# Kernel optimization log

Hardware: AMD Instinct MI355X
Metric: run time of the kernel (lower is better)

## Reference

```python
import jax, jax.numpy as jnp
import numpy as np

N_NODES = 256
IN_FEATURES = 4096
OUT_FEATURES = 7
LAYERS = 4
WIRES = 8                      # ceil(log2(n_nodes))
DIM = 2 ** WIRES               # state-vector length = 256
P2 = WIRES * (WIRES - 1) // 2  # 28 controlled gates per block
N_W = 6 * WIRES + 3 * P2       # 132 weights per layer (matches weight_shape)
CPLX = jnp.complex64
# op2_all_layers ordering: gaps 1..w-1, then j
PAIRS = [(j, j + gap) for gap in range(1, WIRES) for j in range(WIRES - gap)]


def _ry(t):
    c, s = jnp.cos(t / 2), jnp.sin(t / 2)
    return jnp.stack([jnp.stack([c, -s]), jnp.stack([s, c])]).astype(CPLX)


def _rx(t):
    c = jnp.cos(t / 2).astype(CPLX)
    s = (-1j * jnp.sin(t / 2)).astype(CPLX)
    return jnp.stack([jnp.stack([c, s]), jnp.stack([s, c])])


def _rz(t):
    z = jnp.zeros((), CPLX)
    return jnp.stack([jnp.stack([jnp.exp(-0.5j * t).astype(CPLX), z]),
                      jnp.stack([z, jnp.exp(0.5j * t).astype(CPLX)])])


# Constant-angle gates (the source passes the integer weight index as the
# controlled-rotation angle, so these are compile-time numpy constants).
def _ry_np(a):
    c, s = np.cos(a / 2), np.sin(a / 2)
    return np.array([[c, -s], [s, c]], np.complex64)


def _rx_np(a):
    c, s = np.cos(a / 2), np.sin(a / 2)
    return np.array([[c, -1j * s], [-1j * s, c]], np.complex64)


def _rz_np(a):
    return np.diag([np.exp(-0.5j * a), np.exp(0.5j * a)]).astype(np.complex64)


def apply_1q(state, M, q):
    # state: [B] + [2]*WIRES; wire q lives on axis q+1 (wire 0 = MSB, PennyLane order)
    s = jnp.moveaxis(state, q + 1, -1)
    s = jnp.einsum('...b,ab->...a', s, M)
    return jnp.moveaxis(s, -1, q + 1)


def apply_c1q(state, M, c, t):
    # controlled gate: apply M on target wire t in the control==1 subspace
    s = jnp.moveaxis(state, (c + 1, t + 1), (-2, -1))
    s1 = jnp.einsum('...b,ab->...a', s[..., 1, :], M)
    s = jnp.stack([s[..., 0, :], s1], axis=-2)
    return jnp.moveaxis(s, (-2, -1), (c + 1, t + 1))


def q_layer(state, wv):
    # Faithful port of the source q_layer, including the quirk that the
    # CRY/CRX/CRZ angles are the integer running weight index (constants).
    wi = 0
    for q in range(WIRES):
        state = apply_1q(state, _ry(wv[wi + q]), q)
    wi += WIRES
    for i, (c, t) in enumerate(PAIRS):
        state = apply_c1q(state, _ry_np(float(wi + i)), c, t)
    wi += P2
    for q in range(WIRES):
        state = apply_1q(state, _ry(wv[wi + q]), q)
    wi += WIRES
    for q in range(WIRES):
        state = apply_1q(state, _rx(wv[wi + q]), q)
    wi += WIRES
    for i, (c, t) in enumerate(PAIRS):
        state = apply_c1q(state, _rx_np(float(wi + i)), c, t)
    wi += P2
    for q in range(WIRES):
        state = apply_1q(state, _rx(wv[wi + q]), q)
    wi += WIRES
    for q in range(WIRES):
        state = apply_1q(state, _rz(wv[wi + q]), q)
    wi += WIRES
    for i, (c, t) in enumerate(PAIRS):
        state = apply_c1q(state, _rz_np(float(wi + i)), c, t)
    wi += P2
    for q in range(WIRES):
        state = apply_1q(state, _rz(wv[wi + q]), q)
    return state


def circuit(samples, qweights):
    # samples: [B, N_NODES] real -> AmplitudeEmbedding(pad_with=0, normalize=True)
    B = samples.shape[0]
    v = samples
    if DIM > N_NODES:
        v = jnp.pad(v, ((0, 0), (0, DIM - N_NODES)))
    v = v / jnp.linalg.norm(v, axis=1, keepdims=True)
    state = v.astype(CPLX).reshape((B,) + (2,) * WIRES)
    layer = jax.checkpoint(q_layer)  # bounds residual memory under AD
    for l in range(LAYERS):
        state = layer(state, qweights[l])
    p = state.real ** 2 + state.imag ** 2  # probabilities, [B] + [2]*WIRES
    zs = []
    for q in range(WIRES):
        axes = tuple(a for a in range(1, WIRES + 1) if a != q + 1)
        m = p.sum(axis=axes)            # [B, 2]
        zs.append(m[:, 0] - m[:, 1])    # <Z_q> = P(0) - P(1)
    return jnp.stack(zs, axis=1)        # [B, WIRES]


def setup_inputs() -> dict:
    key = jax.random.key(0)
    k1, k2, k3, k4 = jax.random.split(key, 4)
    x = jax.random.normal(k1, (N_NODES, IN_FEATURES), jnp.float32)
    qweights = jax.random.uniform(k2, (LAYERS, N_W), jnp.float32, 0.0, 2.0 * np.pi)
    fc_w = jax.random.normal(k3, (OUT_FEATURES, WIRES), jnp.float32) / np.sqrt(WIRES)
    fc_b = jax.random.normal(k4, (OUT_FEATURES,), jnp.float32) / np.sqrt(WIRES)
    return {"x": x, "qweights": qweights, "fc_w": fc_w, "fc_b": fc_b}


def reference(x, qweights, fc_w, fc_b):
    z = circuit(x.T, qweights)      # [IN_FEATURES, WIRES]
    return z @ fc_w.T + fc_b        # [IN_FEATURES, OUT_FEATURES]
```

## Files before the change

kernel.cpp:

```cpp
#include <hip/hip_runtime.h>
#include <math.h>


namespace {

constexpr int NSAMP = 4096;
constexpr int NW_L  = 132;

constexpr double PI_D   = 3.14159265358979323846264338327950288;
constexpr double TWO_PI = 6.28318530717958647692528676655900577;

constexpr double red_pm_pi(double x) {
  double k = x / TWO_PI;
  long long ki = (long long)k;
  double r = x - (double)ki * TWO_PI;
  if (r > PI_D)  r -= TWO_PI;
  if (r < -PI_D) r += TWO_PI;
  return r;
}
constexpr double csin(double x) {
  double r = red_pm_pi(x), r2 = r * r, term = r, sum = r;
  for (int n = 1; n <= 13; ++n) { term *= -r2 / (double)((2*n)*(2*n+1)); sum += term; }
  return sum;
}
constexpr double ccos(double x) {
  double r = red_pm_pi(x), r2 = r * r, term = 1.0, sum = 1.0;
  for (int n = 1; n <= 13; ++n) { term *= -r2 / (double)((2*n-1)*(2*n)); sum += term; }
  return sum;
}

constexpr int PC[28] = {0,1,2,3,4,5,6, 0,1,2,3,4,5, 0,1,2,3,4, 0,1,2,3, 0,1,2, 0,1, 0};
constexpr int PT[28] = {1,2,3,4,5,6,7, 2,3,4,5,6,7, 3,4,5,6,7, 4,5,6,7, 5,6,7, 6,7, 7};

struct Tbl28 { float c[28]; float s[28]; };
constexpr Tbl28 mk_tbl(int base) {
  Tbl28 t{};
  for (int i = 0; i < 28; ++i) {
    double a = 0.5 * (double)(base + i);
    t.c[i] = (float)ccos(a);
    t.s[i] = (float)csin(a);
  }
  return t;
}
constexpr Tbl28 T_CRY = mk_tbl(8);
constexpr Tbl28 T_CRX = mk_tbl(52);

struct DTbl { float v[512]; };
constexpr DTbl mk_dcrz() {
  DTbl t{};
  for (int s = 0; s < 256; ++s) {
    double psi = 0.0;
    for (int i = 0; i < 28; ++i) {
      const int pc = 7 - PC[i], pt = 7 - PT[i];
      if ((s >> pc) & 1) {
        const double half = 0.5 * (double)(96 + i);
        psi += ((s >> pt) & 1) ? half : -half;
      }
    }
    t.v[2*s]   = (float)ccos(psi);
    t.v[2*s+1] = (float)csin(psi);
  }
  return t;
}
__device__ constexpr DTbl D_CRZ = mk_dcrz();

__device__ __forceinline__ void gen_cross(float* ar, float* ai, int lane, int sh,
                                          float m00r, float m00i, float m01r, float m01i) {
  const int lm = 1 << sh;
  const int bbit = (lane >> sh) & 1;
  const float dr = m00r;
  const float di = bbit ? -m00i : m00i;
  const float g  = bbit ? -m01r : m01r;
  const float h  = m01i;
#pragma unroll
  for (int r = 0; r < 4; ++r) {
    float pr = __shfl_xor(ar[r], lm, 64);
    float pi = __shfl_xor(ai[r], lm, 64);
    float mr = ar[r], mi = ai[r];
    ar[r] = dr*mr - di*mi + g*pr - h*pi;
    ai[r] = dr*mi + di*mr + g*pi + h*pr;
  }
}
__device__ __forceinline__ void gen_local(float* ar, float* ai, int p,
                                          float m00r, float m00i, float m01r, float m01i) {
  const int m = 1 << p;
#pragma unroll
  for (int r0 = 0; r0 < 4; ++r0) {
    if (!(r0 & m)) {
      const int r1 = r0 | m;
      float a0r=ar[r0], a0i=ai[r0], a1r=ar[r1], a1i=ai[r1];
      ar[r0] =  m00r*a0r - m00i*a0i + m01r*a1r - m01i*a1i;
      ai[r0] =  m00r*a0i + m00i*a0r + m01r*a1i + m01i*a1r;
      ar[r1] = -m01r*a0r - m01i*a0i + m00r*a1r + m00i*a1i;
      ai[r1] = -m01r*a0i + m01i*a0r + m00r*a1i - m00i*a1r;
    }
  }
}
__device__ __forceinline__ void cry_cross(float* ar, float* ai, int lane,
                                          int shc, int sht, float cc, float sc) {
  const int lm = 1 << sht;
  const int ctrl = (lane >> shc) & 1;
  const float ce = ctrl ? cc : 1.0f;
  float se = ((lane >> sht) & 1) ? sc : -sc;
  se = ctrl ? se : 0.0f;
#pragma unroll
  for (int r = 0; r < 4; ++r) {
    float pr = __shfl_xor(ar[r], lm, 64);
    float pi = __shfl_xor(ai[r], lm, 64);
    ar[r] = ce*ar[r] + se*pr;
    ai[r] = ce*ai[r] + se*pi;
  }
}
__device__ __forceinline__ void cry_local(float* ar, float* ai, int lane,
                                          int shc, int pt, float cc, float sc) {
  const int ctrl = (lane >> shc) & 1;
  const float ce = ctrl ? cc : 1.0f;
  const float se = ctrl ? sc : 0.0f;
  const int m = 1 << pt;
#pragma unroll
  for (int r0 = 0; r0 < 4; ++r0) {
    if (!(r0 & m)) {
      const int r1 = r0 | m;
      float a0r=ar[r0], a0i=ai[r0], a1r=ar[r1], a1i=ai[r1];
      ar[r0] = ce*a0r - se*a1r;  ai[r0] = ce*a0i - se*a1i;
      ar[r1] = ce*a1r + se*a0r;  ai[r1] = ce*a1i + se*a0i;
    }
  }
}
__device__ __forceinline__ void ry_pair23(float* ar, float* ai, float cc, float sc) {
  float a0r=ar[2], a0i=ai[2], a1r=ar[3], a1i=ai[3];
  ar[2] = cc*a0r - sc*a1r;  ai[2] = cc*a0i - sc*a1i;
  ar[3] = cc*a1r + sc*a0r;  ai[3] = cc*a1i + sc*a0i;
}
__device__ __forceinline__ void crx_cross(float* ar, float* ai, int lane,
                                          int shc, int sht, float cc, float sc) {
  const int lm = 1 << sht;
  const int ctrl = (lane >> shc) & 1;
  const float ce = ctrl ? cc : 1.0f;
  const float se = ctrl ? sc : 0.0f;
#pragma unroll
  for (int r = 0; r < 4; ++r) {
    float pr = __shfl_xor(ar[r], lm, 64);
    float pi = __shfl_xor(ai[r], lm, 64);
    ar[r] = ce*ar[r] + se*pi;
    ai[r] = ce*ai[r] - se*pr;
  }
}
__device__ __forceinline__ void crx_local(float* ar, float* ai, int lane,
                                          int shc, int pt, float cc, float sc) {
  const int ctrl = (lane >> shc) & 1;
  const float ce = ctrl ? cc : 1.0f;
  const float se = ctrl ? sc : 0.0f;
  const int m = 1 << pt;
#pragma unroll
  for (int r0 = 0; r0 < 4; ++r0) {
    if (!(r0 & m)) {
      const int r1 = r0 | m;
      float a0r=ar[r0], a0i=ai[r0], a1r=ar[r1], a1i=ai[r1];
      ar[r0] = ce*a0r + se*a1i;  ai[r0] = ce*a0i - se*a1r;
      ar[r1] = ce*a1r + se*a0i;  ai[r1] = ce*a1i - se*a0r;
    }
  }
}
__device__ __forceinline__ void rx_pair23(float* ar, float* ai, float cc, float sc) {
  float a0r=ar[2], a0i=ai[2], a1r=ar[3], a1i=ai[3];
  ar[2] = cc*a0r + sc*a1i;  ai[2] = cc*a0i - sc*a1r;
  ar[3] = cc*a1r + sc*a0i;  ai[3] = cc*a1i - sc*a0r;
}

__device__ __forceinline__ unsigned short f2bf(float f) {
  unsigned int u = __float_as_uint(f);
  u = (u + 0x7FFFu + ((u >> 16) & 1u)) >> 16;
  return (unsigned short)u;
}

typedef __attribute__((ext_vector_type(8))) short bf16x8;
typedef __attribute__((ext_vector_type(4))) float f32x4;

}

__global__ __launch_bounds__(64) void build_half(const float* __restrict__ qw,
                                                 float* __restrict__ U1c,
                                                 float* __restrict__ U2c) {
  __shared__ float4 sM[48];
  const int lane = threadIdx.x;
  const int h    = blockIdx.x >> 8;
  const int s0   = blockIdx.x & 255;

  if (lane < 48) {
    const int lp  = lane / 24;
    const int rem = lane - lp * 24;
    const int j   = rem >> 3;
    const int q   = rem & 7;
    const int l   = 2 * h + lp;
    float a, bb;
    if (j == 0) {
      a  = qw[l * NW_L + q];
      bb = (l > 0) ? qw[(l - 1) * NW_L + 124 + q] : 0.f;
    } else if (j == 1) {
      a  = qw[l * NW_L + 44 + q];
      bb = qw[l * NW_L + 36 + q];
    } else {
      a  = (l < 3) ? qw[l * NW_L + 88 + q] : 0.f;
      bb = qw[l * NW_L + 80 + q];
    }
    float sa, ca, sb, cb;
    __sincosf(0.5f * a,  &sa, &ca);
    __sincosf(0.5f * bb, &sb, &cb);
    float4 m;
    if (j == 0)      m = make_float4(ca*cb, -ca*sb, -sa*cb, -sa*sb);
    else if (j == 1) m = make_float4(ca*cb, -sa*sb, -ca*sb, -sa*cb);
    else             m = make_float4(ca*cb, -sa*cb, -sb*sa, -sb*ca);
    sM[lane] = m;
  }

  float ar[4], ai[4];
#pragma unroll
  for (int r = 0; r < 4; ++r) {
    ar[r] = (((lane << 2) | r) == s0) ? 1.f : 0.f;
    ai[r] = 0.f;
  }
  float dzr[4], dzi[4];
#pragma unroll
  for (int r = 0; r < 4; ++r) {
    const int s = (lane << 2) | r;
    dzr[r] = D_CRZ.v[2*s];
    dzi[r] = D_CRZ.v[2*s+1];
  }
  __syncthreads();

#pragma unroll 1
  for (int lp = 0; lp < 2; ++lp) {
    const int base = lp * 24;
#pragma unroll
    for (int q = 0; q < 8; ++q) {
      float4 m = sM[base + q];
      if (q <= 5) gen_cross(ar, ai, lane, 5 - q, m.x, m.y, m.z, m.w);
      else        gen_local(ar, ai, 7 - q, m.x, m.y, m.z, m.w);
    }
#pragma unroll
    for (int i = 0; i < 28; ++i) {
      const int c = PC[i], t = PT[i];
      const float cc = T_CRY.c[i], sc = T_CRY.s[i];
      if (t <= 5)      cry_cross(ar, ai, lane, 5 - c, 5 - t, cc, sc);
      else if (c <= 5) cry_local(ar, ai, lane, 5 - c, 7 - t, cc, sc);
      else             ry_pair23(ar, ai, cc, sc);
    }
#pragma unroll
    for (int q = 0; q < 8; ++q) {
      float4 m = sM[base + 8 + q];
      if (q <= 5) gen_cross(ar, ai, lane, 5 - q, m.x, m.y, m.z, m.w);
      else        gen_local(ar, ai, 7 - q, m.x, m.y, m.z, m.w);
    }
#pragma unroll
    for (int i = 0; i < 28; ++i) {
      const int c = PC[i], t = PT[i];
      const float cc = T_CRX.c[i], sc = T_CRX.s[i];
      if (t <= 5)      crx_cross(ar, ai, lane, 5 - c, 5 - t, cc, sc);
      else if (c <= 5) crx_local(ar, ai, lane, 5 - c, 7 - t, cc, sc);
      else             rx_pair23(ar, ai, cc, sc);
    }
#pragma unroll
    for (int q = 0; q < 8; ++q) {
      float4 m = sM[base + 16 + q];
      if (q <= 5) gen_cross(ar, ai, lane, 5 - q, m.x, m.y, m.z, m.w);
      else        gen_local(ar, ai, 7 - q, m.x, m.y, m.z, m.w);
    }
    if (2 * h + lp < 3) {
#pragma unroll
      for (int r = 0; r < 4; ++r) {
        float mr = ar[r], mi = ai[r];
        ar[r] = mr*dzr[r] - mi*dzi[r];
        ai[r] = mr*dzi[r] + mi*dzr[r];
      }
    }
  }

  float* Uc = h ? U2c : U1c;
  float4* dst = (float4*)(Uc + (size_t)s0 * 512);
  dst[2*lane]     = make_float4(ar[0], ai[0], ar[1], ai[1]);
  dst[2*lane + 1] = make_float4(ar[2], ai[2], ar[3], ai[3]);
}

__global__ __launch_bounds__(256) void combine_u(const float* __restrict__ U1c,
                                                 const float* __restrict__ U2c,
                                                 unsigned short* __restrict__ Ubf) {
  __shared__ float2 S2[32 * 16];
  __shared__ float2 S1[16 * 33];
  const int tid = threadIdx.x;
  const int ti  = tid & 15;
  const int tj  = tid >> 4;
  const int bi  = blockIdx.x & 15;
  const int bj  = blockIdx.x >> 4;

  float accr = 0.f, acci = 0.f;
#pragma unroll 1
  for (int kt = 0; kt < 8; ++kt) {
    __syncthreads();
#pragma unroll
    for (int v = 0; v < 2; ++v) {
      const int s = v * 256 + tid;
      const int k  = s >> 4, i = s & 15;
      S2[k * 16 + i] = *(const float2*)(U2c + (size_t)(kt*32 + k) * 512 + (bi*16 + i) * 2);
      const int j2 = s >> 5, k2 = s & 31;
      S1[j2 * 33 + k2] = *(const float2*)(U1c + (size_t)(bj*16 + j2) * 512 + (kt*32 + k2) * 2);
    }
    __syncthreads();
#pragma unroll
    for (int kk = 0; kk < 32; ++kk) {
      const float2 a = S2[kk * 16 + ti];
      const float2 b = S1[tj * 33 + kk];
      accr = fmaf(a.x, b.x, accr);  accr = fmaf(-a.y, b.y, accr);
      acci = fmaf(a.x, b.y, acci);  acci = fmaf(a.y, b.x, acci);
    }
  }
  const int i = bi * 16 + ti, j = bj * 16 + tj;
  Ubf[(size_t)i * 256 + j]         = f2bf(accr);
  Ubf[(size_t)(i + 256) * 256 + j] = f2bf(acci);
}

__global__ __launch_bounds__(256) void mfma_eval(const float* __restrict__ x,
                                                 const unsigned short* __restrict__ Ubf,
                                                 const float* __restrict__ fcw,
                                                 const float* __restrict__ fcb,
                                                 float* __restrict__ out) {
  __shared__ unsigned short Xs[16 * 264];
  __shared__ float Zp[4][16][9];
  __shared__ float Zf[16][9];
  const int tid  = threadIdx.x;
  const int lane = tid & 63;
  const int w    = tid >> 6;
  const int colbase = blockIdx.x * 16;

#pragma unroll
  for (int pass = 0; pass < 16; ++pass) {
    const int k = pass * 16 + (tid >> 4);
    const int c = tid & 15;
    Xs[c * 264 + k] = f2bf(x[(size_t)k * NSAMP + colbase + c]);
  }
  __syncthreads();

  const int quad = lane >> 4;
  const int n    = lane & 15;
  f32x4 acc[8];
#pragma unroll
  for (int rt = 0; rt < 8; ++rt) acc[rt] = (f32x4){0.f, 0.f, 0.f, 0.f};
  const int rowb = w * 128;

#pragma unroll
  for (int kt = 0; kt < 8; ++kt) {
    const bf16x8 bfrag = *(const bf16x8*)&Xs[n * 264 + kt * 32 + quad * 8];
#pragma unroll
    for (int rt = 0; rt < 8; ++rt) {
      const int row = rowb + rt * 16 + n;
      const bf16x8 afrag = *(const bf16x8*)(Ubf + (size_t)row * 256 + kt * 32 + quad * 8);
      acc[rt] = __builtin_amdgcn_mfma_f32_16x16x32_bf16(afrag, bfrag, acc[rt], 0, 0, 0);
    }
  }

  float za[9];
#pragma unroll
  for (int i = 0; i < 9; ++i) za[i] = 0.f;
  const float m4 = (lane & 32) ? -1.f : 1.f;
  const float m5 = (lane & 16) ? -1.f : 1.f;
#pragma unroll
  for (int rt = 0; rt < 8; ++rt) {
#pragma unroll
    for (int reg = 0; reg < 4; ++reg) {
      const float v = acc[rt][reg];
      const float p = v * v;
      za[0] += p;
      za[1] += (w  & 1) ? -p : p;
      za[2] += (rt & 4) ? -p : p;
      za[3] += (rt & 2) ? -p : p;
      za[4] += (rt & 1) ? -p : p;
      za[5] = fmaf(m4, p, za[5]);
      za[6] = fmaf(m5, p, za[6]);
      za[7] += (reg & 2) ? -p : p;
      za[8] += (reg & 1) ? -p : p;
    }
  }
#pragma unroll
  for (int off = 16; off <= 32; off <<= 1) {
#pragma unroll
    for (int i = 0; i < 9; ++i) za[i] += __shfl_xor(za[i], off, 64);
  }
  if (lane < 16) {
#pragma unroll
    for (int i = 0; i < 9; ++i) Zp[w][lane][i] = za[i];
  }
  __syncthreads();

  if (tid < 144) {
    const int col = tid / 9, q = tid - col * 9;
    Zf[col][q] = Zp[0][col][q] + Zp[1][col][q] + Zp[2][col][q] + Zp[3][col][q];
  }
  __syncthreads();

  if (tid < 112) {
    const int col = tid / 7, oo = tid - col * 7;
    const float inv = 1.f / Zf[col][0];
    float v = fcb[oo];
#pragma unroll
    for (int q = 0; q < 8; ++q)
      v = fmaf(fcw[oo * 8 + q], Zf[col][1 + q] * inv, v);
    out[(size_t)(colbase + col) * 7 + oo] = v;
  }
}

extern "C" void kernel_launch(void* const* d_in, const int* in_sizes, int n_in,
                              void* d_out, int out_size, void* d_ws, size_t ws_size,
                              hipStream_t stream) {
  const float* x   = (const float*)d_in[0];
  const float* qw  = (const float*)d_in[1];
  const float* fcw = (const float*)d_in[2];
  const float* fcb = (const float*)d_in[3];
  float* out = (float*)d_out;

  float* U1c = (float*)d_ws;
  float* U2c = U1c + 256 * 512;
  unsigned short* Ubf = (unsigned short*)(U2c + 256 * 512);

  hipLaunchKernelGGL(build_half, dim3(512), dim3(64),  0, stream, qw, U1c, U2c);
  hipLaunchKernelGGL(combine_u,  dim3(256), dim3(256), 0, stream, U1c, U2c, Ubf);
  hipLaunchKernelGGL(mfma_eval,  dim3(256), dim3(256), 0, stream, x, Ubf, fcw, fcb, out);
}
```

Before: 98.75 us.

## Build per-layer unitaries in parallel and combine with a tree of complex GEMMs

The unitary build now simulates one layer per block instead of two layers in sequence, launching 1024 blocks rather than 512. The four layer unitaries are merged pairwise by a new complex-GEMM kernel, then a final GEMM merges the two results. This halves the serial gate-application chain per block and raises parallelism, at the cost of an extra kernel launch, an extra 256^3 complex GEMM and more workspace traffic. Separately, the x-tile load in mfma_eval now uses float4 vector loads.

```diff
diff --git a/kernel.cpp b/kernel.cpp
--- a/kernel.cpp
+++ b/kernel.cpp
@@ -177,22 +177,48 @@
 typedef __attribute__((ext_vector_type(8))) short bf16x8;
 typedef __attribute__((ext_vector_type(4))) float f32x4;
 
-}
-
-__global__ __launch_bounds__(64) void build_half(const float* __restrict__ qw,
-                                                 float* __restrict__ U1c,
-                                                 float* __restrict__ U2c) {
-  __shared__ float4 sM[48];
+__device__ __forceinline__ void cgemm_tile(const float* __restrict__ bufA,
+                                           const float* __restrict__ bufB,
+                                           int bi, int bj, int tid,
+                                           float& accr, float& acci,
+                                           float2* S2 , float2* S1 ) {
+  const int ti = tid & 15;
+  const int tj = tid >> 4;
+  accr = 0.f; acci = 0.f;
+#pragma unroll 1
+  for (int kt = 0; kt < 8; ++kt) {
+    __syncthreads();
+#pragma unroll
+    for (int v = 0; v < 2; ++v) {
+      const int s = v * 256 + tid;
+      const int k = s >> 4, i = s & 15;
+      S2[k * 16 + i] = *(const float2*)(bufA + (size_t)(kt*32 + k) * 512 + (bi*16 + i) * 2);
+      const int j2 = s >> 5, k2 = s & 31;
+      S1[j2 * 33 + k2] = *(const float2*)(bufB + (size_t)(bj*16 + j2) * 512 + (kt*32 + k2) * 2);
+    }
+    __syncthreads();
+#pragma unroll
+    for (int kk = 0; kk < 32; ++kk) {
+      const float2 a = S2[kk * 16 + ti];
+      const float2 b = S1[tj * 33 + kk];
+      accr = fmaf(a.x, b.x, accr);  accr = fmaf(-a.y, b.y, accr);
+      acci = fmaf(a.x, b.y, acci);  acci = fmaf(a.y, b.x, acci);
+    }
+  }
+}
+
+}
+
+__global__ __launch_bounds__(64) void build_quarter(const float* __restrict__ qw,
+                                                    float* __restrict__ Uq) {
+  __shared__ float4 sM[24];
   const int lane = threadIdx.x;
-  const int h    = blockIdx.x >> 8;
+  const int l    = blockIdx.x >> 8;
   const int s0   = blockIdx.x & 255;
 
-  if (lane < 48) {
-    const int lp  = lane / 24;
-    const int rem = lane - lp * 24;
-    const int j   = rem >> 3;
-    const int q   = rem & 7;
-    const int l   = 2 * h + lp;
+  if (lane < 24) {
+    const int j = lane >> 3;
+    const int q = lane & 7;
     float a, bb;
     if (j == 0) {
       a  = qw[l * NW_L + q];
@@ -229,92 +255,83 @@
   }
   __syncthreads();
 
-#pragma unroll 1
-  for (int lp = 0; lp < 2; ++lp) {
-    const int base = lp * 24;
-#pragma unroll
-    for (int q = 0; q < 8; ++q) {
-      float4 m = sM[base + q];
-      if (q <= 5) gen_cross(ar, ai, lane, 5 - q, m.x, m.y, m.z, m.w);
-      else        gen_local(ar, ai, 7 - q, m.x, m.y, m.z, m.w);
-    }
-#pragma unroll
-    for (int i = 0; i < 28; ++i) {
-      const int c = PC[i], t = PT[i];
-      const float cc = T_CRY.c[i], sc = T_CRY.s[i];
-      if (t <= 5)      cry_cross(ar, ai, lane, 5 - c, 5 - t, cc, sc);
-      else if (c <= 5) cry_local(ar, ai, lane, 5 - c, 7 - t, cc, sc);
-      else             ry_pair23(ar, ai, cc, sc);
-    }
-#pragma unroll
-    for (int q = 0; q < 8; ++q) {
-      float4 m = sM[base + 8 + q];
-      if (q <= 5) gen_cross(ar, ai, lane, 5 - q, m.x, m.y, m.z, m.w);
-      else        gen_local(ar, ai, 7 - q, m.x, m.y, m.z, m.w);
-    }
-#pragma unroll
-    for (int i = 0; i < 28; ++i) {
-      const int c = PC[i], t = PT[i];
-      const float cc = T_CRX.c[i], sc = T_CRX.s[i];
-      if (t <= 5)      crx_cross(ar, ai, lane, 5 - c, 5 - t, cc, sc);
-      else if (c <= 5) crx_local(ar, ai, lane, 5 - c, 7 - t, cc, sc);
-      else             rx_pair23(ar, ai, cc, sc);
-    }
-#pragma unroll
-    for (int q = 0; q < 8; ++q) {
-      float4 m = sM[base + 16 + q];
-      if (q <= 5) gen_cross(ar, ai, lane, 5 - q, m.x, m.y, m.z, m.w);
-      else        gen_local(ar, ai, 7 - q, m.x, m.y, m.z, m.w);
-    }
-    if (2 * h + lp < 3) {
-#pragma unroll
-      for (int r = 0; r < 4; ++r) {
-        float mr = ar[r], mi = ai[r];
-        ar[r] = mr*dzr[r] - mi*dzi[r];
-        ai[r] = mr*dzi[r] + mi*dzr[r];
-      }
-    }
-  }
-
-  float* Uc = h ? U2c : U1c;
-  float4* dst = (float4*)(Uc + (size_t)s0 * 512);
+#pragma unroll
+  for (int q = 0; q < 8; ++q) {
+    float4 m = sM[q];
+    if (q <= 5) gen_cross(ar, ai, lane, 5 - q, m.x, m.y, m.z, m.w);
+    else        gen_local(ar, ai, 7 - q, m.x, m.y, m.z, m.w);
+  }
+#pragma unroll
+  for (int i = 0; i < 28; ++i) {
+    const int c = PC[i], t = PT[i];
+    const float cc = T_CRY.c[i], sc = T_CRY.s[i];
+    if (t <= 5)      cry_cross(ar, ai, lane, 5 - c, 5 - t, cc, sc);
+    else if (c <= 5) cry_local(ar, ai, lane, 5 - c, 7 - t, cc, sc);
+    else             ry_pair23(ar, ai, cc, sc);
+  }
+#pragma unroll
+  for (int q = 0; q < 8; ++q) {
+    float4 m = sM[8 + q];
+    if (q <= 5) gen_cross(ar, ai, lane, 5 - q, m.x, m.y, m.z, m.w);
+    else        gen_local(ar, ai, 7 - q, m.x, m.y, m.z, m.w);
+  }
+#pragma unroll
+  for (int i = 0; i < 28; ++i) {
+    const int c = PC[i], t = PT[i];
+    const float cc = T_CRX.c[i], sc = T_CRX.s[i];
+    if (t <= 5)      crx_cross(ar, ai, lane, 5 - c, 5 - t, cc, sc);
+    else if (c <= 5) crx_local(ar, ai, lane, 5 - c, 7 - t, cc, sc);
+    else             rx_pair23(ar, ai, cc, sc);
+  }
+#pragma unroll
+  for (int q = 0; q < 8; ++q) {
+    float4 m = sM[16 + q];
+    if (q <= 5) gen_cross(ar, ai, lane, 5 - q, m.x, m.y, m.z, m.w);
+    else        gen_local(ar, ai, 7 - q, m.x, m.y, m.z, m.w);
+  }
+  if (l < 3) {
+#pragma unroll
+    for (int r = 0; r < 4; ++r) {
+      float mr = ar[r], mi = ai[r];
+      ar[r] = mr*dzr[r] - mi*dzi[r];
+      ai[r] = mr*dzi[r] + mi*dzr[r];
+    }
+  }
+
+  float4* dst = (float4*)(Uq + (size_t)(l * 256 + s0) * 512);
   dst[2*lane]     = make_float4(ar[0], ai[0], ar[1], ai[1]);
   dst[2*lane + 1] = make_float4(ar[2], ai[2], ar[3], ai[3]);
 }
 
-__global__ __launch_bounds__(256) void combine_u(const float* __restrict__ U1c,
-                                                 const float* __restrict__ U2c,
-                                                 unsigned short* __restrict__ Ubf) {
+__global__ __launch_bounds__(256) void combine_pair(const float* __restrict__ Uq,
+                                                    float* __restrict__ Tc) {
   __shared__ float2 S2[32 * 16];
   __shared__ float2 S1[16 * 33];
   const int tid = threadIdx.x;
-  const int ti  = tid & 15;
-  const int tj  = tid >> 4;
+  const int p   = blockIdx.x >> 8;
+  const int rem = blockIdx.x & 255;
+  const int bi  = rem & 15;
+  const int bj  = rem >> 4;
+  const float* bufA = Uq + (size_t)(2*p + 1) * 256 * 512;
+  const float* bufB = Uq + (size_t)(2*p) * 256 * 512;
+  float accr, acci;
+  cgemm_tile(bufA, bufB, bi, bj, tid, accr, acci, S2, S1);
+  const int i = bi * 16 + (tid & 15), j = bj * 16 + (tid >> 4);
+  *(float2*)(Tc + (size_t)p * 256 * 512 + (size_t)j * 512 + i * 2) = make_float2(accr, acci);
+}
+
+__global__ __launch_bounds__(256) void combine_final(const float* __restrict__ Tc,
+                                                     unsigned short* __restrict__ Ubf) {
+  __shared__ float2 S2[32 * 16];
+  __shared__ float2 S1[16 * 33];
+  const int tid = threadIdx.x;
   const int bi  = blockIdx.x & 15;
   const int bj  = blockIdx.x >> 4;
-
-  float accr = 0.f, acci = 0.f;
-#pragma unroll 1
-  for (int kt = 0; kt < 8; ++kt) {
-    __syncthreads();
-#pragma unroll
-    for (int v = 0; v < 2; ++v) {
-      const int s = v * 256 + tid;
-      const int k  = s >> 4, i = s & 15;
-      S2[k * 16 + i] = *(const float2*)(U2c + (size_t)(kt*32 + k) * 512 + (bi*16 + i) * 2);
-      const int j2 = s >> 5, k2 = s & 31;
-      S1[j2 * 33 + k2] = *(const float2*)(U1c + (size_t)(bj*16 + j2) * 512 + (kt*32 + k2) * 2);
-    }
-    __syncthreads();
-#pragma unroll
-    for (int kk = 0; kk < 32; ++kk) {
-      const float2 a = S2[kk * 16 + ti];
-      const float2 b = S1[tj * 33 + kk];
-      accr = fmaf(a.x, b.x, accr);  accr = fmaf(-a.y, b.y, accr);
-      acci = fmaf(a.x, b.y, acci);  acci = fmaf(a.y, b.x, acci);
-    }
-  }
-  const int i = bi * 16 + ti, j = bj * 16 + tj;
+  const float* bufA = Tc + (size_t)256 * 512;
+  const float* bufB = Tc;
+  float accr, acci;
+  cgemm_tile(bufA, bufB, bi, bj, tid, accr, acci, S2, S1);
+  const int i = bi * 16 + (tid & 15), j = bj * 16 + (tid >> 4);
   Ubf[(size_t)i * 256 + j]         = f2bf(accr);
   Ubf[(size_t)(i + 256) * 256 + j] = f2bf(acci);
 }
@@ -333,10 +350,14 @@
   const int colbase = blockIdx.x * 16;
 
 #pragma unroll
-  for (int pass = 0; pass < 16; ++pass) {
-    const int k = pass * 16 + (tid >> 4);
-    const int c = tid & 15;
-    Xs[c * 264 + k] = f2bf(x[(size_t)k * NSAMP + colbase + c]);
+  for (int pass = 0; pass < 4; ++pass) {
+    const int k  = pass * 64 + (tid >> 2);
+    const int c4 = (tid & 3) * 4;
+    const float4 v = *(const float4*)(x + (size_t)k * NSAMP + colbase + c4);
+    Xs[(c4 + 0) * 264 + k] = f2bf(v.x);
+    Xs[(c4 + 1) * 264 + k] = f2bf(v.y);
+    Xs[(c4 + 2) * 264 + k] = f2bf(v.z);
+    Xs[(c4 + 3) * 264 + k] = f2bf(v.w);
   }
   __syncthreads();
 
@@ -417,11 +438,12 @@
   const float* fcb = (const float*)d_in[3];
   float* out = (float*)d_out;
 
-  float* U1c = (float*)d_ws;
-  float* U2c = U1c + 256 * 512;
-  unsigned short* Ubf = (unsigned short*)(U2c + 256 * 512);
-
-  hipLaunchKernelGGL(build_half, dim3(512), dim3(64),  0, stream, qw, U1c, U2c);
-  hipLaunchKernelGGL(combine_u,  dim3(256), dim3(256), 0, stream, U1c, U2c, Ubf);
-  hipLaunchKernelGGL(mfma_eval,  dim3(256), dim3(256), 0, stream, x, Ubf, fcw, fcb, out);
-}
+  float* Uq = (float*)d_ws;
+  float* Tc = Uq + (size_t)4 * 256 * 512;
+  unsigned short* Ubf = (unsigned short*)(Tc + (size_t)2 * 256 * 512);
+
+  hipLaunchKernelGGL(build_quarter, dim3(1024), dim3(64),  0, stream, qw, Uq);
+  hipLaunchKernelGGL(combine_pair,  dim3(512),  dim3(256), 0, stream, Uq, Tc);
+  hipLaunchKernelGGL(combine_final, dim3(256),  dim3(256), 0, stream, Tc, Ubf);
+  hipLaunchKernelGGL(mfma_eval,     dim3(256),  dim3(256), 0, stream, x, Ubf, fcw, fcb, out);
+}
```

Result: slower. 101.4 us (+2.7%).

## Drop U2·U1 combine kernel; apply two half-unitaries in sequence inside eval

Applied to the files above, without the earlier changes.

Removes the combine_u kernel that multiplied the two half-circuit unitaries. Instead, build_half2 writes U1 and a real-embedded W2 directly in bf16, and eval2 applies them as two chained MFMA GEMMs with the intermediate state held in shared memory. It also swaps xor-shuffles for DPP at small strides and vectorises the x load. This saves one launch and the fp32 256x256 complex matmul, but adds MFMA work per column block and an extra bf16 rounding of the intermediate state.

```diff
diff --git a/kernel.cpp b/kernel.cpp
--- a/kernel.cpp
+++ b/kernel.cpp
@@ -64,9 +64,22 @@
 }
 __device__ constexpr DTbl D_CRZ = mk_dcrz();
 
+__device__ __forceinline__ float shx(float v, int sh) {
+  if (sh == 0) {
+    int r = __builtin_amdgcn_update_dpp((int)__float_as_uint(v), (int)__float_as_uint(v),
+                                        0xB1, 0xF, 0xF, true);
+    return __uint_as_float((unsigned)r);
+  }
+  if (sh == 1) {
+    int r = __builtin_amdgcn_update_dpp((int)__float_as_uint(v), (int)__float_as_uint(v),
+                                        0x4E, 0xF, 0xF, true);
+    return __uint_as_float((unsigned)r);
+  }
+  return __shfl_xor(v, 1 << sh, 64);
+}
+
 __device__ __forceinline__ void gen_cross(float* ar, float* ai, int lane, int sh,
                                           float m00r, float m00i, float m01r, float m01i) {
-  const int lm = 1 << sh;
   const int bbit = (lane >> sh) & 1;
   const float dr = m00r;
   const float di = bbit ? -m00i : m00i;
@@ -74,8 +87,8 @@
   const float h  = m01i;
 #pragma unroll
   for (int r = 0; r < 4; ++r) {
-    float pr = __shfl_xor(ar[r], lm, 64);
-    float pi = __shfl_xor(ai[r], lm, 64);
+    float pr = shx(ar[r], sh);
+    float pi = shx(ai[r], sh);
     float mr = ar[r], mi = ai[r];
     ar[r] = dr*mr - di*mi + g*pr - h*pi;
     ai[r] = dr*mi + di*mr + g*pi + h*pr;
@@ -98,15 +111,14 @@
 }
 __device__ __forceinline__ void cry_cross(float* ar, float* ai, int lane,
                                           int shc, int sht, float cc, float sc) {
-  const int lm = 1 << sht;
   const int ctrl = (lane >> shc) & 1;
   const float ce = ctrl ? cc : 1.0f;
   float se = ((lane >> sht) & 1) ? sc : -sc;
   se = ctrl ? se : 0.0f;
 #pragma unroll
   for (int r = 0; r < 4; ++r) {
-    float pr = __shfl_xor(ar[r], lm, 64);
-    float pi = __shfl_xor(ai[r], lm, 64);
+    float pr = shx(ar[r], sht);
+    float pi = shx(ai[r], sht);
     ar[r] = ce*ar[r] + se*pr;
     ai[r] = ce*ai[r] + se*pi;
   }
@@ -134,14 +146,13 @@
 }
 __device__ __forceinline__ void crx_cross(float* ar, float* ai, int lane,
                                           int shc, int sht, float cc, float sc) {
-  const int lm = 1 << sht;
   const int ctrl = (lane >> shc) & 1;
   const float ce = ctrl ? cc : 1.0f;
   const float se = ctrl ? sc : 0.0f;
 #pragma unroll
   for (int r = 0; r < 4; ++r) {
-    float pr = __shfl_xor(ar[r], lm, 64);
-    float pi = __shfl_xor(ai[r], lm, 64);
+    float pr = shx(ar[r], sht);
+    float pi = shx(ai[r], sht);
     ar[r] = ce*ar[r] + se*pi;
     ai[r] = ce*ai[r] - se*pr;
   }
@@ -179,20 +190,24 @@
 
 }
 
-__global__ __launch_bounds__(64) void build_half(const float* __restrict__ qw,
-                                                 float* __restrict__ U1c,
-                                                 float* __restrict__ U2c) {
-  __shared__ float4 sM[48];
-  const int lane = threadIdx.x;
-  const int h    = blockIdx.x >> 8;
-  const int s0   = blockIdx.x & 255;
-
-  if (lane < 48) {
-    const int lp  = lane / 24;
-    const int rem = lane - lp * 24;
+__global__ __launch_bounds__(512) void build_half2(const float* __restrict__ qw,
+                                                   unsigned short* __restrict__ U1bf,
+                                                   unsigned short* __restrict__ W2bf) {
+  __shared__ float4 sM[96];
+  __shared__ float Lre[2][4][256];
+  __shared__ float Lim[2][4][256];
+  const int tid  = threadIdx.x;
+  const int lane = tid & 63;
+  const int w    = tid >> 6;
+  const int h    = w >> 2;
+  const int c    = w & 3;
+  const int s0   = blockIdx.x * 4 + c;
+
+  if (tid < 96) {
+    const int l   = tid / 24;
+    const int rem = tid - l * 24;
     const int j   = rem >> 3;
     const int q   = rem & 7;
-    const int l   = 2 * h + lp;
     float a, bb;
     if (j == 0) {
       a  = qw[l * NW_L + q];
@@ -211,7 +226,7 @@
     if (j == 0)      m = make_float4(ca*cb, -ca*sb, -sa*cb, -sa*sb);
     else if (j == 1) m = make_float4(ca*cb, -sa*sb, -ca*sb, -sa*cb);
     else             m = make_float4(ca*cb, -sa*cb, -sb*sa, -sb*ca);
-    sM[lane] = m;
+    sM[tid] = m;
   }
 
   float ar[4], ai[4];
@@ -231,7 +246,8 @@
 
 #pragma unroll 1
   for (int lp = 0; lp < 2; ++lp) {
-    const int base = lp * 24;
+    const int l    = 2 * h + lp;
+    const int base = l * 24;
 #pragma unroll
     for (int q = 0; q < 8; ++q) {
       float4 m = sM[base + q];
@@ -240,11 +256,11 @@
     }
 #pragma unroll
     for (int i = 0; i < 28; ++i) {
-      const int c = PC[i], t = PT[i];
-      const float cc = T_CRY.c[i], sc = T_CRY.s[i];
-      if (t <= 5)      cry_cross(ar, ai, lane, 5 - c, 5 - t, cc, sc);
-      else if (c <= 5) cry_local(ar, ai, lane, 5 - c, 7 - t, cc, sc);
-      else             ry_pair23(ar, ai, cc, sc);
+      const int cc_ = PC[i], t = PT[i];
+      const float gc = T_CRY.c[i], gs = T_CRY.s[i];
+      if (t <= 5)       cry_cross(ar, ai, lane, 5 - cc_, 5 - t, gc, gs);
+      else if (cc_ <= 5) cry_local(ar, ai, lane, 5 - cc_, 7 - t, gc, gs);
+      else              ry_pair23(ar, ai, gc, gs);
     }
 #pragma unroll
     for (int q = 0; q < 8; ++q) {
@@ -254,11 +270,11 @@
     }
 #pragma unroll
     for (int i = 0; i < 28; ++i) {
-      const int c = PC[i], t = PT[i];
-      const float cc = T_CRX.c[i], sc = T_CRX.s[i];
-      if (t <= 5)      crx_cross(ar, ai, lane, 5 - c, 5 - t, cc, sc);
-      else if (c <= 5) crx_local(ar, ai, lane, 5 - c, 7 - t, cc, sc);
-      else             rx_pair23(ar, ai, cc, sc);
+      const int cc_ = PC[i], t = PT[i];
+      const float gc = T_CRX.c[i], gs = T_CRX.s[i];
+      if (t <= 5)       crx_cross(ar, ai, lane, 5 - cc_, 5 - t, gc, gs);
+      else if (cc_ <= 5) crx_local(ar, ai, lane, 5 - cc_, 7 - t, gc, gs);
+      else              rx_pair23(ar, ai, gc, gs);
     }
 #pragma unroll
     for (int q = 0; q < 8; ++q) {
@@ -266,7 +282,7 @@
       if (q <= 5) gen_cross(ar, ai, lane, 5 - q, m.x, m.y, m.z, m.w);
       else        gen_local(ar, ai, 7 - q, m.x, m.y, m.z, m.w);
     }
-    if (2 * h + lp < 3) {
+    if (l < 3) {
 #pragma unroll
       for (int r = 0; r < 4; ++r) {
         float mr = ar[r], mi = ai[r];
@@ -276,55 +292,41 @@
     }
   }
 
-  float* Uc = h ? U2c : U1c;
-  float4* dst = (float4*)(Uc + (size_t)s0 * 512);
-  dst[2*lane]     = make_float4(ar[0], ai[0], ar[1], ai[1]);
-  dst[2*lane + 1] = make_float4(ar[2], ai[2], ar[3], ai[3]);
-}
-
-__global__ __launch_bounds__(256) void combine_u(const float* __restrict__ U1c,
-                                                 const float* __restrict__ U2c,
-                                                 unsigned short* __restrict__ Ubf) {
-  __shared__ float2 S2[32 * 16];
-  __shared__ float2 S1[16 * 33];
-  const int tid = threadIdx.x;
-  const int ti  = tid & 15;
-  const int tj  = tid >> 4;
-  const int bi  = blockIdx.x & 15;
-  const int bj  = blockIdx.x >> 4;
-
-  float accr = 0.f, acci = 0.f;
-#pragma unroll 1
-  for (int kt = 0; kt < 8; ++kt) {
-    __syncthreads();
-#pragma unroll
-    for (int v = 0; v < 2; ++v) {
-      const int s = v * 256 + tid;
-      const int k  = s >> 4, i = s & 15;
-      S2[k * 16 + i] = *(const float2*)(U2c + (size_t)(kt*32 + k) * 512 + (bi*16 + i) * 2);
-      const int j2 = s >> 5, k2 = s & 31;
-      S1[j2 * 33 + k2] = *(const float2*)(U1c + (size_t)(bj*16 + j2) * 512 + (kt*32 + k2) * 2);
-    }
-    __syncthreads();
-#pragma unroll
-    for (int kk = 0; kk < 32; ++kk) {
-      const float2 a = S2[kk * 16 + ti];
-      const float2 b = S1[tj * 33 + kk];
-      accr = fmaf(a.x, b.x, accr);  accr = fmaf(-a.y, b.y, accr);
-      acci = fmaf(a.x, b.y, acci);  acci = fmaf(a.y, b.x, acci);
-    }
-  }
-  const int i = bi * 16 + ti, j = bj * 16 + tj;
-  Ubf[(size_t)i * 256 + j]         = f2bf(accr);
-  Ubf[(size_t)(i + 256) * 256 + j] = f2bf(acci);
-}
-
-__global__ __launch_bounds__(256) void mfma_eval(const float* __restrict__ x,
-                                                 const unsigned short* __restrict__ Ubf,
-                                                 const float* __restrict__ fcw,
-                                                 const float* __restrict__ fcb,
-                                                 float* __restrict__ out) {
+#pragma unroll
+  for (int r = 0; r < 4; ++r) {
+    const int s = (lane << 2) | r;
+    Lre[h][c][s] = ar[r];
+    Lim[h][c][s] = ai[r];
+  }
+  __syncthreads();
+
+  {
+    const int r = tid;
+    const int cb = blockIdx.x * 4;
+    unsigned short u1[4], wa[4], wb[4];
+#pragma unroll
+    for (int k = 0; k < 4; ++k) {
+      const float v1 = (r < 256) ? Lre[0][k][r] : Lim[0][k][r - 256];
+      u1[k] = f2bf(v1);
+      const float va = (r < 256) ? Lre[1][k][r] : Lim[1][k][r - 256];
+      wa[k] = f2bf(va);
+      const float vb = (r < 256) ? -Lim[1][k][r] : Lre[1][k][r - 256];
+      wb[k] = f2bf(vb);
+    }
+    *(uint2*)(U1bf + (size_t)r * 256 + cb)       = *(const uint2*)u1;
+    *(uint2*)(W2bf + (size_t)r * 512 + cb)       = *(const uint2*)wa;
+    *(uint2*)(W2bf + (size_t)r * 512 + 256 + cb) = *(const uint2*)wb;
+  }
+}
+
+__global__ __launch_bounds__(256) void eval2(const float* __restrict__ x,
+                                             const unsigned short* __restrict__ U1bf,
+                                             const unsigned short* __restrict__ W2bf,
+                                             const float* __restrict__ fcw,
+                                             const float* __restrict__ fcb,
+                                             float* __restrict__ out) {
   __shared__ unsigned short Xs[16 * 264];
+  __shared__ unsigned short Ys[16 * 520];
   __shared__ float Zp[4][16][9];
   __shared__ float Zf[16][9];
   const int tid  = threadIdx.x;
@@ -333,27 +335,55 @@
   const int colbase = blockIdx.x * 16;
 
 #pragma unroll
-  for (int pass = 0; pass < 16; ++pass) {
-    const int k = pass * 16 + (tid >> 4);
-    const int c = tid & 15;
-    Xs[c * 264 + k] = f2bf(x[(size_t)k * NSAMP + colbase + c]);
+  for (int pass = 0; pass < 4; ++pass) {
+    const int k  = pass * 64 + (tid >> 2);
+    const int c4 = (tid & 3) * 4;
+    const float4 v = *(const float4*)(x + (size_t)k * NSAMP + colbase + c4);
+    Xs[(c4 + 0) * 264 + k] = f2bf(v.x);
+    Xs[(c4 + 1) * 264 + k] = f2bf(v.y);
+    Xs[(c4 + 2) * 264 + k] = f2bf(v.z);
+    Xs[(c4 + 3) * 264 + k] = f2bf(v.w);
   }
   __syncthreads();
 
   const int quad = lane >> 4;
   const int n    = lane & 15;
+  const int rowb = w * 128;
+
+  {
+    f32x4 acc[8];
+#pragma unroll
+    for (int rt = 0; rt < 8; ++rt) acc[rt] = (f32x4){0.f, 0.f, 0.f, 0.f};
+#pragma unroll
+    for (int kt = 0; kt < 8; ++kt) {
+      const bf16x8 bfrag = *(const bf16x8*)&Xs[n * 264 + kt * 32 + quad * 8];
+#pragma unroll
+      for (int rt = 0; rt < 8; ++rt) {
+        const int row = rowb + rt * 16 + n;
+        const bf16x8 afrag = *(const bf16x8*)(U1bf + (size_t)row * 256 + kt * 32 + quad * 8);
+        acc[rt] = __builtin_amdgcn_mfma_f32_16x16x32_bf16(afrag, bfrag, acc[rt], 0, 0, 0);
+      }
+    }
+#pragma unroll
+    for (int rt = 0; rt < 8; ++rt) {
+      unsigned short p4[4];
+#pragma unroll
+      for (int reg = 0; reg < 4; ++reg) p4[reg] = f2bf(acc[rt][reg]);
+      *(uint2*)&Ys[n * 520 + rowb + rt * 16 + quad * 4] = *(const uint2*)p4;
+    }
+  }
+  __syncthreads();
+
   f32x4 acc[8];
 #pragma unroll
   for (int rt = 0; rt < 8; ++rt) acc[rt] = (f32x4){0.f, 0.f, 0.f, 0.f};
-  const int rowb = w * 128;
-
-#pragma unroll
-  for (int kt = 0; kt < 8; ++kt) {
-    const bf16x8 bfrag = *(const bf16x8*)&Xs[n * 264 + kt * 32 + quad * 8];
+#pragma unroll
+  for (int kt = 0; kt < 16; ++kt) {
+    const bf16x8 bfrag = *(const bf16x8*)&Ys[n * 520 + kt * 32 + quad * 8];
 #pragma unroll
     for (int rt = 0; rt < 8; ++rt) {
       const int row = rowb + rt * 16 + n;
-      const bf16x8 afrag = *(const bf16x8*)(Ubf + (size_t)row * 256 + kt * 32 + quad * 8);
+      const bf16x8 afrag = *(const bf16x8*)(W2bf + (size_t)row * 512 + kt * 32 + quad * 8);
       acc[rt] = __builtin_amdgcn_mfma_f32_16x16x32_bf16(afrag, bfrag, acc[rt], 0, 0, 0);
     }
   }
@@ -417,11 +447,10 @@
   const float* fcb = (const float*)d_in[3];
   float* out = (float*)d_out;
 
-  float* U1c = (float*)d_ws;
-  float* U2c = U1c + 256 * 512;
-  unsigned short* Ubf = (unsigned short*)(U2c + 256 * 512);
-
-  hipLaunchKernelGGL(build_half, dim3(512), dim3(64),  0, stream, qw, U1c, U2c);
-  hipLaunchKernelGGL(combine_u,  dim3(256), dim3(256), 0, stream, U1c, U2c, Ubf);
-  hipLaunchKernelGGL(mfma_eval,  dim3(256), dim3(256), 0, stream, x, Ubf, fcw, fcb, out);
-}
+  unsigned short* U1bf = (unsigned short*)d_ws;
+  unsigned short* W2bf = U1bf + (size_t)512 * 256;
+
+  hipLaunchKernelGGL(build_half2, dim3(64),  dim3(512), 0, stream, qw, U1bf, W2bf);
+  hipLaunchKernelGGL(eval2,       dim3(256), dim3(256), 0, stream,
+                     x, U1bf, W2bf, fcw, fcb, out);
+}
```

Result: slower. 116.1 us (+17.6%).

## Use DPP lane swaps for short shuffles and widen eval to 16 waves

Applied to the files above, without the earlier changes.

Cross-lane swaps at distance 1 and 2 now use DPP quad permutes instead of ds_bpermute-based shuffles in the circuit-building kernels. The eval kernel grows from 4 to 16 waves per block, each wave owning 32 rows of the unitary instead of 128, and the input tile is loaded with float4 reads. The per-wave partial Z sums are reduced over 16 waves instead of 4. The aim is lower shuffle latency and more parallelism and latency hiding in the MFMA stage, at the cost of more shared-memory reduction and larger blocks.

```diff
diff --git a/kernel.cpp b/kernel.cpp
--- a/kernel.cpp
+++ b/kernel.cpp
@@ -64,9 +64,22 @@
 }
 __device__ constexpr DTbl D_CRZ = mk_dcrz();
 
+__device__ __forceinline__ float shx(float v, int sh) {
+  if (sh == 0) {
+    int r = __builtin_amdgcn_update_dpp((int)__float_as_uint(v), (int)__float_as_uint(v),
+                                        0xB1, 0xF, 0xF, true);
+    return __uint_as_float((unsigned)r);
+  }
+  if (sh == 1) {
+    int r = __builtin_amdgcn_update_dpp((int)__float_as_uint(v), (int)__float_as_uint(v),
+                                        0x4E, 0xF, 0xF, true);
+    return __uint_as_float((unsigned)r);
+  }
+  return __shfl_xor(v, 1 << sh, 64);
+}
+
 __device__ __forceinline__ void gen_cross(float* ar, float* ai, int lane, int sh,
                                           float m00r, float m00i, float m01r, float m01i) {
-  const int lm = 1 << sh;
   const int bbit = (lane >> sh) & 1;
   const float dr = m00r;
   const float di = bbit ? -m00i : m00i;
@@ -74,8 +87,8 @@
   const float h  = m01i;
 #pragma unroll
   for (int r = 0; r < 4; ++r) {
-    float pr = __shfl_xor(ar[r], lm, 64);
-    float pi = __shfl_xor(ai[r], lm, 64);
+    float pr = shx(ar[r], sh);
+    float pi = shx(ai[r], sh);
     float mr = ar[r], mi = ai[r];
     ar[r] = dr*mr - di*mi + g*pr - h*pi;
     ai[r] = dr*mi + di*mr + g*pi + h*pr;
@@ -98,15 +111,14 @@
 }
 __device__ __forceinline__ void cry_cross(float* ar, float* ai, int lane,
                                           int shc, int sht, float cc, float sc) {
-  const int lm = 1 << sht;
   const int ctrl = (lane >> shc) & 1;
   const float ce = ctrl ? cc : 1.0f;
   float se = ((lane >> sht) & 1) ? sc : -sc;
   se = ctrl ? se : 0.0f;
 #pragma unroll
   for (int r = 0; r < 4; ++r) {
-    float pr = __shfl_xor(ar[r], lm, 64);
-    float pi = __shfl_xor(ai[r], lm, 64);
+    float pr = shx(ar[r], sht);
+    float pi = shx(ai[r], sht);
     ar[r] = ce*ar[r] + se*pr;
     ai[r] = ce*ai[r] + se*pi;
   }
@@ -134,14 +146,13 @@
 }
 __device__ __forceinline__ void crx_cross(float* ar, float* ai, int lane,
                                           int shc, int sht, float cc, float sc) {
-  const int lm = 1 << sht;
   const int ctrl = (lane >> shc) & 1;
   const float ce = ctrl ? cc : 1.0f;
   const float se = ctrl ? sc : 0.0f;
 #pragma unroll
   for (int r = 0; r < 4; ++r) {
-    float pr = __shfl_xor(ar[r], lm, 64);
-    float pi = __shfl_xor(ai[r], lm, 64);
+    float pr = shx(ar[r], sht);
+    float pi = shx(ai[r], sht);
     ar[r] = ce*ar[r] + se*pi;
     ai[r] = ce*ai[r] - se*pr;
   }
@@ -319,39 +330,43 @@
   Ubf[(size_t)(i + 256) * 256 + j] = f2bf(acci);
 }
 
-__global__ __launch_bounds__(256) void mfma_eval(const float* __restrict__ x,
-                                                 const unsigned short* __restrict__ Ubf,
-                                                 const float* __restrict__ fcw,
-                                                 const float* __restrict__ fcb,
-                                                 float* __restrict__ out) {
+__global__ __launch_bounds__(1024) void eval3(const float* __restrict__ x,
+                                              const unsigned short* __restrict__ Ubf,
+                                              const float* __restrict__ fcw,
+                                              const float* __restrict__ fcb,
+                                              float* __restrict__ out) {
   __shared__ unsigned short Xs[16 * 264];
-  __shared__ float Zp[4][16][9];
+  __shared__ float Zp[16][16][9];
   __shared__ float Zf[16][9];
   const int tid  = threadIdx.x;
   const int lane = tid & 63;
   const int w    = tid >> 6;
   const int colbase = blockIdx.x * 16;
 
-#pragma unroll
-  for (int pass = 0; pass < 16; ++pass) {
-    const int k = pass * 16 + (tid >> 4);
-    const int c = tid & 15;
-    Xs[c * 264 + k] = f2bf(x[(size_t)k * NSAMP + colbase + c]);
+  {
+    const int k  = tid >> 2;
+    const int c4 = (tid & 3) * 4;
+    const float4 v = *(const float4*)(x + (size_t)k * NSAMP + colbase + c4);
+    Xs[(c4 + 0) * 264 + k] = f2bf(v.x);
+    Xs[(c4 + 1) * 264 + k] = f2bf(v.y);
+    Xs[(c4 + 2) * 264 + k] = f2bf(v.z);
+    Xs[(c4 + 3) * 264 + k] = f2bf(v.w);
   }
   __syncthreads();
 
   const int quad = lane >> 4;
   const int n    = lane & 15;
-  f32x4 acc[8];
-#pragma unroll
-  for (int rt = 0; rt < 8; ++rt) acc[rt] = (f32x4){0.f, 0.f, 0.f, 0.f};
-  const int rowb = w * 128;
+  const int rowb = w * 32;
+
+  f32x4 acc[2];
+  acc[0] = (f32x4){0.f, 0.f, 0.f, 0.f};
+  acc[1] = (f32x4){0.f, 0.f, 0.f, 0.f};
 
 #pragma unroll
   for (int kt = 0; kt < 8; ++kt) {
     const bf16x8 bfrag = *(const bf16x8*)&Xs[n * 264 + kt * 32 + quad * 8];
 #pragma unroll
-    for (int rt = 0; rt < 8; ++rt) {
+    for (int rt = 0; rt < 2; ++rt) {
       const int row = rowb + rt * 16 + n;
       const bf16x8 afrag = *(const bf16x8*)(Ubf + (size_t)row * 256 + kt * 32 + quad * 8);
       acc[rt] = __builtin_amdgcn_mfma_f32_16x16x32_bf16(afrag, bfrag, acc[rt], 0, 0, 0);
@@ -364,16 +379,16 @@
   const float m4 = (lane & 32) ? -1.f : 1.f;
   const float m5 = (lane & 16) ? -1.f : 1.f;
 #pragma unroll
-  for (int rt = 0; rt < 8; ++rt) {
+  for (int rt = 0; rt < 2; ++rt) {
 #pragma unroll
     for (int reg = 0; reg < 4; ++reg) {
       const float v = acc[rt][reg];
       const float p = v * v;
       za[0] += p;
-      za[1] += (w  & 1) ? -p : p;
-      za[2] += (rt & 4) ? -p : p;
-      za[3] += (rt & 2) ? -p : p;
-      za[4] += (rt & 1) ? -p : p;
+      za[1] += (w & 4)   ? -p : p;
+      za[2] += (w & 2)   ? -p : p;
+      za[3] += (w & 1)   ? -p : p;
+      za[4] += rt        ? -p : p;
       za[5] = fmaf(m4, p, za[5]);
       za[6] = fmaf(m5, p, za[6]);
       za[7] += (reg & 2) ? -p : p;
@@ -393,7 +408,10 @@
 
   if (tid < 144) {
     const int col = tid / 9, q = tid - col * 9;
-    Zf[col][q] = Zp[0][col][q] + Zp[1][col][q] + Zp[2][col][q] + Zp[3][col][q];
+    float z = 0.f;
+#pragma unroll
+    for (int ww = 0; ww < 16; ++ww) z += Zp[ww][col][q];
+    Zf[col][q] = z;
   }
   __syncthreads();
 
@@ -421,7 +439,7 @@
   float* U2c = U1c + 256 * 512;
   unsigned short* Ubf = (unsigned short*)(U2c + 256 * 512);
 
-  hipLaunchKernelGGL(build_half, dim3(512), dim3(64),  0, stream, qw, U1c, U2c);
-  hipLaunchKernelGGL(combine_u,  dim3(256), dim3(256), 0, stream, U1c, U2c, Ubf);
-  hipLaunchKernelGGL(mfma_eval,  dim3(256), dim3(256), 0, stream, x, Ubf, fcw, fcb, out);
-}
+  hipLaunchKernelGGL(build_half, dim3(512), dim3(64),   0, stream, qw, U1c, U2c);
+  hipLaunchKernelGGL(combine_u,  dim3(256), dim3(256),  0, stream, U1c, U2c, Ubf);
+  hipLaunchKernelGGL(eval3,      dim3(256), dim3(1024), 0, stream, x, Ubf, fcw, fcb, out);
+}
```

Measured after the change: 94.84 us. 4.0% less time.
